# Performance work log

Hardware: AMD Instinct MI355X
Metric: run time of the kernel (lower is better)

The kernel has to match this reference:

```python
import jax, jax.numpy as jnp
import numpy as np

N = 100000
E = 1600000
IN_DIM = 256
HID = 128


def setup_inputs() -> dict:
    key = jax.random.key(0)
    k = jax.random.split(key, 8)
    x = jax.random.normal(k[0], (N, IN_DIM), dtype=jnp.float32)
    edge_index = jax.random.randint(k[1], (2, E), 0, N, dtype=jnp.int64 if jax.config.jax_enable_x64 else jnp.int32)
    # GCNConv weight (no bias pre-aggregation; bias added after aggregation, as in PyG)
    W_conv = jax.random.normal(k[2], (IN_DIM, HID), dtype=jnp.float32) / np.sqrt(IN_DIM)
    b_conv = jnp.zeros((HID,), dtype=jnp.float32)
    prelu_a = jnp.full((1,), 0.25, dtype=jnp.float32)  # torch.nn.PReLU default init
    W_lin = jax.random.normal(k[3], (HID, IN_DIM), dtype=jnp.float32) / np.sqrt(HID)
    b_lin = jnp.zeros((IN_DIM,), dtype=jnp.float32)
    return {"x": x, "edge_index": edge_index, "W_conv": W_conv, "b_conv": b_conv,
            "prelu_a": prelu_a, "W_lin": W_lin, "b_lin": b_lin}


def _gcn_conv(x, edge_index, W, b):
    # h = x @ W  ([N, HID])
    h = x @ W
    src, dst = edge_index[0], edge_index[1]
    # add self-loops
    loops = jnp.arange(N, dtype=src.dtype)
    src = jnp.concatenate([src, loops])
    dst = jnp.concatenate([dst, loops])
    # symmetric degree normalization deg^-1/2 (degree over incoming edges incl. self-loops)
    deg = jax.ops.segment_sum(jnp.ones_like(dst, dtype=h.dtype), dst, num_segments=N)
    dinv = jnp.where(deg > 0, jax.lax.rsqrt(deg), 0.0)
    norm = dinv[src] * dinv[dst]                     # [E+N]
    msg = h[src] * norm[:, None]                     # gather + scale  [E+N, HID]
    out = jax.ops.segment_sum(msg, dst, num_segments=N)  # scatter-add  [N, HID]
    return out + b


def reference(x, edge_index, W_conv, b_conv, prelu_a, W_lin, b_lin):
    h = _gcn_conv(x, edge_index, W_conv, b_conv)
    h = jnp.where(h >= 0, h, prelu_a * h)            # PReLU (single shared slope)
    # dropout p=0.0 -> identity
    return h @ W_lin + b_lin                          # [N, IN_DIM]
```

## Files before the change

### kernel.cpp

```cpp
#include <hip/hip_runtime.h>

#define N_NODES 100000
#define E_EDGES 1600000
#define INDIM 256
#define HID 128
#define CAP 48
#define NPART 8
#define PART_SZ 12500
#define ECAP 32768
#define PA_BLOCKS 1563
#define PA_STRIDE (PA_BLOCKS * 256)
#define G1_BLOCKS 1563
#define PB_BLOCKS 1024

typedef __attribute__((ext_vector_type(8))) short s16x8;
typedef __attribute__((ext_vector_type(4))) float f32x4;
typedef __attribute__((ext_vector_type(4))) unsigned int u32x4;

__device__ __forceinline__ unsigned short cvt_bf16(float f) {
    unsigned int u = __float_as_uint(f);
    u += 0x7FFFu + ((u >> 16) & 1u);
    return (unsigned short)(u >> 16);
}
__device__ __forceinline__ float bf16_to_f(unsigned short s) {
    return __uint_as_float(((unsigned int)s) << 16);
}

__global__ __launch_bounds__(256) void prepzero_kernel(const float* __restrict__ Wc,
                                                       const float* __restrict__ Wl,
                                                       unsigned short* __restrict__ f1,
                                                       unsigned short* __restrict__ f2,
                                                       int* __restrict__ count) {
    const int b = blockIdx.x;
    const int tid = threadIdx.x;
    if (b < 256) {
        int pt = b * 256 + tid;
        if (pt < 32768) {
            int j = pt & 7, L = (pt >> 3) & 63, t = (pt >> 9) & 7, c = pt >> 12;
            int k = c * 32 + ((L >> 4) * 8) + j;
            int n = t * 16 + (L & 15);
            f1[pt] = cvt_bf16(Wc[k * 128 + n]);
        } else {
            int u = pt - 32768;
            int j = u & 7, L = (u >> 3) & 63, t = (u >> 9) & 15, c = u >> 13;
            int k = c * 32 + ((L >> 4) * 8) + j;
            int n = t * 16 + (L & 15);
            f2[u] = cvt_bf16(Wl[k * 256 + n]);
        }
    } else {
        for (int i = (b - 256) * 256 + tid; i < 100352; i += 256 * 256) count[i] = 0;
    }
}

__global__ __launch_bounds__(256) void fata_kernel(const int* __restrict__ src,
                                                   const int* __restrict__ dst,
                                                   int* __restrict__ gcnt,
                                                   unsigned int* __restrict__ pedges,
                                                   const float* __restrict__ x,
                                                   const unsigned short* __restrict__ fragW,
                                                   unsigned short* __restrict__ h) {
    __shared__ __align__(16) unsigned short xs[64 * 48];
    __shared__ int sCount[8];
    __shared__ int sBase[8];
    const int tid = threadIdx.x;

    if (blockIdx.x < PA_BLOCKS) {
        if (tid < 8) sCount[tid] = 0;
        __syncthreads();
        const int lane = tid & 63;
        const int t0 = blockIdx.x * 256 + tid;
        const int xcd = blockIdx.x & 7;

        unsigned int pk[4];
        int pp[4];
        int lo[4];
#pragma unroll
        for (int r = 0; r < 4; ++r) {
            int e = t0 + r * PA_STRIDE;
            bool valid = e < E_EDGES;
            int d = 0, s = 0;
            if (valid) {
                d = __builtin_nontemporal_load(dst + e);
                s = __builtin_nontemporal_load(src + e);
            }
            int p = valid ? d / PART_SZ : 8;
            unsigned long long mask_p = 0ull;
#pragma unroll
            for (int v = 0; v < 8; ++v) {
                unsigned long long mv = __ballot(p == v);
                if (p == v) mask_p = mv;
            }
            int off = __popcll(mask_p & ((1ull << lane) - 1ull));
            int ldr = (mask_p == 0ull) ? 0 : (__ffsll(mask_p) - 1);
            int wbase = 0;
            if (valid && lane == ldr) wbase = atomicAdd(&sCount[p], __popcll(mask_p));
            wbase = __shfl(wbase, ldr);
            pp[r] = p;
            lo[r] = wbase + off;
            pk[r] = ((unsigned int)(d - p * PART_SZ) << 17) | (unsigned int)s;
        }
        __syncthreads();
        if (tid < 8) sBase[tid] = atomicAdd(&gcnt[xcd * 8 + tid], sCount[tid]);
        __syncthreads();
#pragma unroll
        for (int r = 0; r < 4; ++r) {
            if (pp[r] < 8) {
                int pos = sBase[pp[r]] + lo[r];
                if (pos < ECAP)
                    pedges[(size_t)(xcd * 8 + pp[r]) * ECAP + pos] = pk[r];
            }
        }
    } else {
        const int r0 = (blockIdx.x - PA_BLOCKS) * 64;
        const int w = tid >> 6, lane = tid & 63;
        const int q = lane >> 4, m = lane & 15;
        const int srow = tid >> 2, skg = tid & 3;

        f32x4 acc[8];
#pragma unroll
        for (int t = 0; t < 8; ++t) acc[t] = (f32x4){0.f, 0.f, 0.f, 0.f};

        const s16x8* fwv = (const s16x8*)fragW;

        for (int c = 0; c < 8; ++c) {
            int gr = r0 + srow;
            f32x4 v0 = (f32x4){0.f, 0.f, 0.f, 0.f}, v1 = v0;
            if (gr < N_NODES) {
                const f32x4* p = (const f32x4*)&x[(size_t)gr * INDIM + c * 32 + skg * 8];
                v0 = __builtin_nontemporal_load(p);
                v1 = __builtin_nontemporal_load(p + 1);
            }
            uint4 pk;
            pk.x = ((unsigned)cvt_bf16(v0.y) << 16) | cvt_bf16(v0.x);
            pk.y = ((unsigned)cvt_bf16(v0.w) << 16) | cvt_bf16(v0.z);
            pk.z = ((unsigned)cvt_bf16(v1.y) << 16) | cvt_bf16(v1.x);
            pk.w = ((unsigned)cvt_bf16(v1.w) << 16) | cvt_bf16(v1.z);
            *(uint4*)&xs[srow * 48 + skg * 8] = pk;
            __syncthreads();

            s16x8 a = *(const s16x8*)&xs[(w * 16 + m) * 48 + q * 8];
#pragma unroll
            for (int t = 0; t < 8; ++t) {
                s16x8 b = fwv[(c * 8 + t) * 64 + lane];
                acc[t] = __builtin_amdgcn_mfma_f32_16x16x32_bf16(a, b, acc[t], 0, 0, 0);
            }
            __syncthreads();
        }

        const int row_base = r0 + w * 16 + q * 4;
#pragma unroll
        for (int t = 0; t < 8; ++t) {
#pragma unroll
            for (int r = 0; r < 4; ++r) {
                int row = row_base + r;
                if (row < N_NODES)
                    __builtin_nontemporal_store(cvt_bf16(acc[t][r]),
                        h + (size_t)row * HID + t * 16 + m);
            }
        }
    }
}

__global__ __launch_bounds__(256) void partb_kernel(const unsigned int* __restrict__ pedges,
                                                    const int* __restrict__ gcnt,
                                                    int* __restrict__ count,
                                                    int* __restrict__ bucket) {
    const int part = blockIdx.x & 7;
    const int bslot = blockIdx.x >> 3;
    const int tid = threadIdx.x;
#pragma unroll
    for (int xx = 0; xx < 8; ++xx) {
        int n = gcnt[xx * 8 + part];
        if (n > ECAP) n = ECAP;
        const unsigned int* lst = pedges + (size_t)(xx * 8 + part) * ECAP;
        for (int i = bslot * 256 + tid; i < n; i += (PB_BLOCKS / 8) * 256) {
            unsigned int v = __builtin_nontemporal_load(lst + i);
            int s = (int)(v & 0x1FFFFu);
            int d = part * PART_SZ + (int)(v >> 17);
            int slot = atomicAdd(&count[d], 1);
            if (slot < CAP) bucket[d * CAP + slot] = s;
        }
    }
}

__device__ __forceinline__ void gather_node(int wid, int lane, int g, int l,
                                            const int* __restrict__ bucket,
                                            const int* __restrict__ count,
                                            const uint4* __restrict__ hp4,
                                            const float* bc, float a,
                                            unsigned int* o) {
    const int raw = count[wid];
    const float dn = rsqrtf((float)(raw + 1));
    int deg = raw > CAP ? CAP : raw;

    int s_l = wid;
    float dv_l = 0.f;
    if (lane < deg) {
        s_l = bucket[wid * CAP + lane];
        dv_l = rsqrtf((float)(count[s_l] + 1));
    }

    float acc[8];
    {
        uint4 hv = hp4[(size_t)wid * 16 + l];
        float w0 = (g == 0) ? dn * dn : 0.f;
        const unsigned int* pv = (const unsigned int*)&hv;
#pragma unroll
        for (int k = 0; k < 4; ++k) {
            acc[2 * k]     = w0 * bf16_to_f((unsigned short)(pv[k] & 0xFFFF));
            acc[2 * k + 1] = w0 * bf16_to_f((unsigned short)(pv[k] >> 16));
        }
    }

    for (int j = 0; j < deg; j += 8) {
        int e0 = j + g;
        int e1 = j + 4 + g;
        int s0 = __shfl(s_l, e0);
        int s1 = __shfl(s_l, e1);
        float w0 = __shfl(dv_l, e0) * dn;
        float w1 = __shfl(dv_l, e1) * dn;
        uint4 hv0 = hp4[(size_t)s0 * 16 + l];
        uint4 hv1 = hp4[(size_t)s1 * 16 + l];
        const unsigned int* p0 = (const unsigned int*)&hv0;
        const unsigned int* p1 = (const unsigned int*)&hv1;
#pragma unroll
        for (int k = 0; k < 4; ++k) {
            acc[2 * k]     += w0 * bf16_to_f((unsigned short)(p0[k] & 0xFFFF));
            acc[2 * k + 1] += w0 * bf16_to_f((unsigned short)(p0[k] >> 16));
        }
#pragma unroll
        for (int k = 0; k < 4; ++k) {
            acc[2 * k]     += w1 * bf16_to_f((unsigned short)(p1[k] & 0xFFFF));
            acc[2 * k + 1] += w1 * bf16_to_f((unsigned short)(p1[k] >> 16));
        }
    }

#pragma unroll
    for (int k = 0; k < 8; ++k) {
        acc[k] += __shfl_xor(acc[k], 16);
        acc[k] += __shfl_xor(acc[k], 32);
    }

#pragma unroll
    for (int k = 0; k < 4; ++k) {
        float ox = acc[2 * k] + bc[2 * k];
        float oy = acc[2 * k + 1] + bc[2 * k + 1];
        ox = ox >= 0.f ? ox : a * ox;
        oy = oy >= 0.f ? oy : a * oy;
        o[k] = ((unsigned)cvt_bf16(oy) << 16) | cvt_bf16(ox);
    }
}

__global__ __launch_bounds__(1024) void gg_kernel(const int* __restrict__ bucket,
                                                  const int* __restrict__ count,
                                                  const unsigned short* __restrict__ h,
                                                  const float* __restrict__ b_conv,
                                                  const float* __restrict__ prelu_a,
                                                  const unsigned short* __restrict__ fragW,
                                                  const float* __restrict__ b_lin,
                                                  float* __restrict__ out) {
    __shared__ __align__(16) unsigned short xs[4 * 64 * 48];
    const int tid = threadIdx.x;
    const int wv = tid >> 6;
    const int lane = tid & 63;
    const int g = lane >> 4;
    const int l = lane & 15;
    const int r0 = blockIdx.x * 64;
    const uint4* hp4 = (const uint4*)h;

    const float a = prelu_a[0];
    float bc[8];
    {
        float4 b0 = *(const float4*)&b_conv[l * 8];
        float4 b1 = *(const float4*)&b_conv[l * 8 + 4];
        bc[0] = b0.x; bc[1] = b0.y; bc[2] = b0.z; bc[3] = b0.w;
        bc[4] = b1.x; bc[5] = b1.y; bc[6] = b1.z; bc[7] = b1.w;
    }

#pragma unroll
    for (int k = 0; k < 4; ++k) {
        const int n = wv * 4 + k;
        const int wid = r0 + n;
        if (wid < N_NODES) {
            unsigned int o[4];
            gather_node(wid, lane, g, l, bucket, count, hp4, bc, a, o);
            if (g == 0) {
                uint4 ov;
                ov.x = o[0]; ov.y = o[1]; ov.z = o[2]; ov.w = o[3];
                *(uint4*)&xs[((l >> 2) * 64 + n) * 48 + (l & 3) * 8] = ov;
            }
        }
    }
    __syncthreads();

    const int q = g, m = l;
    const int rg = wv & 3;
    const int cg = wv >> 2;
    f32x4 acc[4];
#pragma unroll
    for (int t = 0; t < 4; ++t) acc[t] = (f32x4){0.f, 0.f, 0.f, 0.f};

    const s16x8* fwv = (const s16x8*)fragW;
#pragma unroll
    for (int c = 0; c < 4; ++c) {
        s16x8 av = *(const s16x8*)&xs[(c * 64 + rg * 16 + m) * 48 + q * 8];
#pragma unroll
        for (int t = 0; t < 4; ++t) {
            s16x8 b = fwv[(c * 16 + cg * 4 + t) * 64 + lane];
            acc[t] = __builtin_amdgcn_mfma_f32_16x16x32_bf16(av, b, acc[t], 0, 0, 0);
        }
    }

    const int row_base = r0 + rg * 16 + q * 4;
#pragma unroll
    for (int t = 0; t < 4; ++t) {
        int col = (cg * 4 + t) * 16 + m;
        float bias = b_lin[col];
#pragma unroll
        for (int r = 0; r < 4; ++r) {
            int row = row_base + r;
            if (row < N_NODES)
                __builtin_nontemporal_store(acc[t][r] + bias,
                    out + (size_t)row * INDIM + col);
        }
    }
}

extern "C" void kernel_launch(void* const* d_in, const int* in_sizes, int n_in,
                              void* d_out, int out_size, void* d_ws, size_t ws_size,
                              hipStream_t stream) {
    const float* x       = (const float*)d_in[0];
    const int*   eidx    = (const int*)d_in[1];
    const float* W_conv  = (const float*)d_in[2];
    const float* b_conv  = (const float*)d_in[3];
    const float* prelu_a = (const float*)d_in[4];
    const float* W_lin   = (const float*)d_in[5];
    const float* b_lin   = (const float*)d_in[6];
    float* out = (float*)d_out;

    const int* src = eidx;
    const int* dst = eidx + E_EDGES;

    char* base = (char*)d_ws;
    const size_t SZ_BUCKET = (size_t)N_NODES * CAP * 4;
    const size_t SZ_H      = (size_t)N_NODES * HID * 2;
    const size_t SZ_PED    = (size_t)64 * ECAP * 4;
    int* bucket = (int*)base;
    unsigned short* h = (unsigned short*)(base + SZ_BUCKET);
    unsigned int* pedges = (unsigned int*)(base + SZ_BUCKET + SZ_H);
    int* count = (int*)(base + SZ_BUCKET + SZ_H + SZ_PED);
    int* gcnt  = count + 100000;
    unsigned short* fragW1 = (unsigned short*)(count + 100352);
    unsigned short* fragW2 = fragW1 + 32768;

    prepzero_kernel<<<512, 256, 0, stream>>>(W_conv, W_lin, fragW1, fragW2, count);

    fata_kernel<<<PA_BLOCKS + G1_BLOCKS, 256, 0, stream>>>(
        src, dst, gcnt, pedges, x, fragW1, h);

    partb_kernel<<<PB_BLOCKS, 256, 0, stream>>>(pedges, gcnt, count, bucket);

    gg_kernel<<<(N_NODES + 63) / 64, 1024, 0, stream>>>(
        bucket, count, h, b_conv, prelu_a, fragW2, b_lin, out);
}
```

Baseline: 397.0 us.

## Regroup pipeline stages: fuse weight prep with edge partitioning, bucketing with GEMM

Kernel boundaries are reshuffled. Weight fragment conversion and count zeroing now share a kernel with edge partitioning, and the first GEMM runs in the same launch as the bucket fill, with a memset zeroing the partition counters beforehand. This removes one launch and lets the scatter-heavy bucketing overlap with the compute-bound GEMM. Bucket capacity grows from 48 to 64, and the gather loop is unrolled to load four neighbor rows per step, which adds memory traffic for the larger bucket array.

```diff
diff --git a/kernel.cpp b/kernel.cpp
--- a/kernel.cpp
+++ b/kernel.cpp
@@ -4,7 +4,7 @@
 #define E_EDGES 1600000
 #define INDIM 256
 #define HID 128
-#define CAP 48
+#define CAP 64
 #define NPART 8
 #define PART_SZ 12500
 #define ECAP 32768
@@ -26,15 +26,21 @@
     return __uint_as_float(((unsigned int)s) << 16);
 }
 
-__global__ __launch_bounds__(256) void prepzero_kernel(const float* __restrict__ Wc,
-                                                       const float* __restrict__ Wl,
-                                                       unsigned short* __restrict__ f1,
-                                                       unsigned short* __restrict__ f2,
-                                                       int* __restrict__ count) {
-    const int b = blockIdx.x;
+__global__ __launch_bounds__(256) void parta_kernel(const int* __restrict__ src,
+                                                    const int* __restrict__ dst,
+                                                    int* __restrict__ gcnt,
+                                                    unsigned int* __restrict__ pedges,
+                                                    const float* __restrict__ Wc,
+                                                    const float* __restrict__ Wl,
+                                                    unsigned short* __restrict__ f1,
+                                                    unsigned short* __restrict__ f2,
+                                                    int* __restrict__ count) {
+    __shared__ int sCount[8];
+    __shared__ int sBase[8];
     const int tid = threadIdx.x;
-    if (b < 256) {
-        int pt = b * 256 + tid;
+
+    if (blockIdx.x < 256) {
+        int pt = blockIdx.x * 256 + tid;
         if (pt < 32768) {
             int j = pt & 7, L = (pt >> 3) & 63, t = (pt >> 9) & 7, c = pt >> 12;
             int k = c * 32 + ((L >> 4) * 8) + j;
@@ -47,71 +53,71 @@
             int n = t * 16 + (L & 15);
             f2[u] = cvt_bf16(Wl[k * 256 + n]);
         }
-    } else {
-        for (int i = (b - 256) * 256 + tid; i < 100352; i += 256 * 256) count[i] = 0;
-    }
-}
-
-__global__ __launch_bounds__(256) void fata_kernel(const int* __restrict__ src,
-                                                   const int* __restrict__ dst,
-                                                   int* __restrict__ gcnt,
-                                                   unsigned int* __restrict__ pedges,
-                                                   const float* __restrict__ x,
-                                                   const unsigned short* __restrict__ fragW,
-                                                   unsigned short* __restrict__ h) {
+    } else if (blockIdx.x < 512) {
+        for (int i = (blockIdx.x - 256) * 256 + tid; i < 100000; i += 256 * 256)
+            count[i] = 0;
+    }
+
+    if (tid < 8) sCount[tid] = 0;
+    __syncthreads();
+    const int lane = tid & 63;
+    const int t0 = blockIdx.x * 256 + tid;
+    const int xcd = blockIdx.x & 7;
+
+    unsigned int pk[4];
+    int pp[4];
+    int lo[4];
+#pragma unroll
+    for (int r = 0; r < 4; ++r) {
+        int e = t0 + r * PA_STRIDE;
+        bool valid = e < E_EDGES;
+        int d = 0, s = 0;
+        if (valid) {
+            d = __builtin_nontemporal_load(dst + e);
+            s = __builtin_nontemporal_load(src + e);
+        }
+        int p = valid ? d / PART_SZ : 8;
+        unsigned long long mask_p = 0ull;
+#pragma unroll
+        for (int v = 0; v < 8; ++v) {
+            unsigned long long mv = __ballot(p == v);
+            if (p == v) mask_p = mv;
+        }
+        int off = __popcll(mask_p & ((1ull << lane) - 1ull));
+        int ldr = (mask_p == 0ull) ? 0 : (__ffsll(mask_p) - 1);
+        int wbase = 0;
+        if (valid && lane == ldr) wbase = atomicAdd(&sCount[p], __popcll(mask_p));
+        wbase = __shfl(wbase, ldr);
+        pp[r] = p;
+        lo[r] = wbase + off;
+        pk[r] = ((unsigned int)(d - p * PART_SZ) << 17) | (unsigned int)s;
+    }
+    __syncthreads();
+    if (tid < 8) sBase[tid] = atomicAdd(&gcnt[xcd * 8 + tid], sCount[tid]);
+    __syncthreads();
+#pragma unroll
+    for (int r = 0; r < 4; ++r) {
+        if (pp[r] < 8) {
+            int pos = sBase[pp[r]] + lo[r];
+            if (pos < ECAP)
+                __builtin_nontemporal_store(pk[r],
+                    pedges + (size_t)(xcd * 8 + pp[r]) * ECAP + pos);
+        }
+    }
+}
+
+__global__ __launch_bounds__(256) void fat_kernel(const float* __restrict__ x,
+                                                  const unsigned short* __restrict__ fragW,
+                                                  unsigned short* __restrict__ h,
+                                                  const unsigned int* __restrict__ pedges,
+                                                  const int* __restrict__ gcnt,
+                                                  int* __restrict__ count,
+                                                  int* __restrict__ bucket) {
     __shared__ __align__(16) unsigned short xs[64 * 48];
-    __shared__ int sCount[8];
-    __shared__ int sBase[8];
     const int tid = threadIdx.x;
 
-    if (blockIdx.x < PA_BLOCKS) {
-        if (tid < 8) sCount[tid] = 0;
-        __syncthreads();
-        const int lane = tid & 63;
-        const int t0 = blockIdx.x * 256 + tid;
-        const int xcd = blockIdx.x & 7;
-
-        unsigned int pk[4];
-        int pp[4];
-        int lo[4];
-#pragma unroll
-        for (int r = 0; r < 4; ++r) {
-            int e = t0 + r * PA_STRIDE;
-            bool valid = e < E_EDGES;
-            int d = 0, s = 0;
-            if (valid) {
-                d = __builtin_nontemporal_load(dst + e);
-                s = __builtin_nontemporal_load(src + e);
-            }
-            int p = valid ? d / PART_SZ : 8;
-            unsigned long long mask_p = 0ull;
-#pragma unroll
-            for (int v = 0; v < 8; ++v) {
-                unsigned long long mv = __ballot(p == v);
-                if (p == v) mask_p = mv;
-            }
-            int off = __popcll(mask_p & ((1ull << lane) - 1ull));
-            int ldr = (mask_p == 0ull) ? 0 : (__ffsll(mask_p) - 1);
-            int wbase = 0;
-            if (valid && lane == ldr) wbase = atomicAdd(&sCount[p], __popcll(mask_p));
-            wbase = __shfl(wbase, ldr);
-            pp[r] = p;
-            lo[r] = wbase + off;
-            pk[r] = ((unsigned int)(d - p * PART_SZ) << 17) | (unsigned int)s;
-        }
-        __syncthreads();
-        if (tid < 8) sBase[tid] = atomicAdd(&gcnt[xcd * 8 + tid], sCount[tid]);
-        __syncthreads();
-#pragma unroll
-        for (int r = 0; r < 4; ++r) {
-            if (pp[r] < 8) {
-                int pos = sBase[pp[r]] + lo[r];
-                if (pos < ECAP)
-                    pedges[(size_t)(xcd * 8 + pp[r]) * ECAP + pos] = pk[r];
-            }
-        }
-    } else {
-        const int r0 = (blockIdx.x - PA_BLOCKS) * 64;
+    if (blockIdx.x < G1_BLOCKS) {
+        const int r0 = blockIdx.x * 64;
         const int w = tid >> 6, lane = tid & 63;
         const int q = lane >> 4, m = lane & 15;
         const int srow = tid >> 2, skg = tid & 3;
@@ -158,27 +164,21 @@
                         h + (size_t)row * HID + t * 16 + m);
             }
         }
-    }
-}
-
-__global__ __launch_bounds__(256) void partb_kernel(const unsigned int* __restrict__ pedges,
-                                                    const int* __restrict__ gcnt,
-                                                    int* __restrict__ count,
-                                                    int* __restrict__ bucket) {
-    const int part = blockIdx.x & 7;
-    const int bslot = blockIdx.x >> 3;
-    const int tid = threadIdx.x;
-#pragma unroll
-    for (int xx = 0; xx < 8; ++xx) {
-        int n = gcnt[xx * 8 + part];
-        if (n > ECAP) n = ECAP;
-        const unsigned int* lst = pedges + (size_t)(xx * 8 + part) * ECAP;
-        for (int i = bslot * 256 + tid; i < n; i += (PB_BLOCKS / 8) * 256) {
-            unsigned int v = __builtin_nontemporal_load(lst + i);
-            int s = (int)(v & 0x1FFFFu);
-            int d = part * PART_SZ + (int)(v >> 17);
-            int slot = atomicAdd(&count[d], 1);
-            if (slot < CAP) bucket[d * CAP + slot] = s;
+    } else {
+        const int part = blockIdx.x & 7;
+        const int bslot = (blockIdx.x - G1_BLOCKS) >> 3;
+#pragma unroll
+        for (int xx = 0; xx < 8; ++xx) {
+            int n = gcnt[xx * 8 + part];
+            if (n > ECAP) n = ECAP;
+            const unsigned int* lst = pedges + (size_t)(xx * 8 + part) * ECAP;
+            for (int i = bslot * 256 + tid; i < n; i += (PB_BLOCKS / 8) * 256) {
+                unsigned int v = __builtin_nontemporal_load(lst + i);
+                int s = (int)(v & 0x1FFFFu);
+                int d = part * PART_SZ + (int)(v >> 17);
+                int slot = atomicAdd(&count[d], 1);
+                if (slot < CAP) bucket[d * CAP + slot] = s;
+            }
         }
     }
 }
@@ -212,17 +212,27 @@
         }
     }
 
-    for (int j = 0; j < deg; j += 8) {
+    for (int j = 0; j < deg; j += 16) {
         int e0 = j + g;
         int e1 = j + 4 + g;
+        int e2 = j + 8 + g;
+        int e3 = j + 12 + g;
         int s0 = __shfl(s_l, e0);
         int s1 = __shfl(s_l, e1);
+        int s2 = __shfl(s_l, e2);
+        int s3 = __shfl(s_l, e3);
         float w0 = __shfl(dv_l, e0) * dn;
         float w1 = __shfl(dv_l, e1) * dn;
+        float w2 = __shfl(dv_l, e2) * dn;
+        float w3 = __shfl(dv_l, e3) * dn;
         uint4 hv0 = hp4[(size_t)s0 * 16 + l];
         uint4 hv1 = hp4[(size_t)s1 * 16 + l];
+        uint4 hv2 = hp4[(size_t)s2 * 16 + l];
+        uint4 hv3 = hp4[(size_t)s3 * 16 + l];
         const unsigned int* p0 = (const unsigned int*)&hv0;
         const unsigned int* p1 = (const unsigned int*)&hv1;
+        const unsigned int* p2 = (const unsigned int*)&hv2;
+        const unsigned int* p3 = (const unsigned int*)&hv3;
 #pragma unroll
         for (int k = 0; k < 4; ++k) {
             acc[2 * k]     += w0 * bf16_to_f((unsigned short)(p0[k] & 0xFFFF));
@@ -232,6 +242,16 @@
         for (int k = 0; k < 4; ++k) {
             acc[2 * k]     += w1 * bf16_to_f((unsigned short)(p1[k] & 0xFFFF));
             acc[2 * k + 1] += w1 * bf16_to_f((unsigned short)(p1[k] >> 16));
+        }
+#pragma unroll
+        for (int k = 0; k < 4; ++k) {
+            acc[2 * k]     += w2 * bf16_to_f((unsigned short)(p2[k] & 0xFFFF));
+            acc[2 * k + 1] += w2 * bf16_to_f((unsigned short)(p2[k] >> 16));
+        }
+#pragma unroll
+        for (int k = 0; k < 4; ++k) {
+            acc[2 * k]     += w3 * bf16_to_f((unsigned short)(p3[k] & 0xFFFF));
+            acc[2 * k + 1] += w3 * bf16_to_f((unsigned short)(p3[k] >> 16));
         }
     }
 
@@ -353,12 +373,13 @@
     unsigned short* fragW1 = (unsigned short*)(count + 100352);
     unsigned short* fragW2 = fragW1 + 32768;
 
-    prepzero_kernel<<<512, 256, 0, stream>>>(W_conv, W_lin, fragW1, fragW2, count);
-
-    fata_kernel<<<PA_BLOCKS + G1_BLOCKS, 256, 0, stream>>>(
-        src, dst, gcnt, pedges, x, fragW1, h);
-
-    partb_kernel<<<PB_BLOCKS, 256, 0, stream>>>(pedges, gcnt, count, bucket);
+    hipMemsetAsync(gcnt, 0, 352 * sizeof(int), stream);
+
+    parta_kernel<<<PA_BLOCKS, 256, 0, stream>>>(src, dst, gcnt, pedges,
+                                                W_conv, W_lin, fragW1, fragW2, count);
+
+    fat_kernel<<<G1_BLOCKS + PB_BLOCKS, 256, 0, stream>>>(x, fragW1, h,
+                                                          pedges, gcnt, count, bucket);
 
     gg_kernel<<<(N_NODES + 63) / 64, 1024, 0, stream>>>(
         bucket, count, h, b_conv, prelu_a, fragW2, b_lin, out);
```

After: 396.9 us. Within noise of the previous version (-0.0%).
